# Performance work log

Hardware: AMD Instinct MI355X
Metric: run time of the kernel (lower is better)

Reference implementation:

```python
import jax, jax.numpy as jnp
import numpy as np

B, NV, NC, D, GD = 4, 2048, 8192, 64, 8


def setup_inputs() -> dict:
    key = jax.random.key(0)
    ks = jax.random.split(key, 16)
    f32 = jnp.float32
    rn = lambda k, s, fan: (jax.random.normal(k, s, dtype=f32) / np.float32(np.sqrt(fan)))
    raw = jax.random.randint(ks[0], (B, NC, NV), 0, 20)
    c_mat = jnp.where(raw == 0, -1.0, jnp.where(raw == 1, 1.0, 0.0)).astype(f32)
    v_mat = jnp.transpose(c_mat, (0, 2, 1))  # [B, NV, NC]
    variables = jax.random.normal(ks[1], (B, NV, D), dtype=f32)
    ground_vars = jax.random.normal(ks[2], (B, NV, GD), dtype=f32)
    # learned params
    c_block = rn(ks[3], (2, D, D), D)  # pos/neg literal projections (clause side)
    v_block = rn(ks[4], (2, D, D), D)  # pos/neg literal projections (variable side)
    vb = jax.random.normal(ks[5], (D,), dtype=f32)
    cb = jax.random.normal(ks[6], (D,), dtype=f32)
    Wg = rn(ks[7], (D, GD + D), GD + D)  # ground combiner Linear(concat) -> D
    bg = jnp.zeros((D,), f32)
    Wz = rn(ks[8], (D, D), D); Uz = rn(ks[9], (D, D), D); bz = jnp.zeros((D,), f32)
    Wr = rn(ks[10], (D, D), D); Ur = rn(ks[11], (D, D), D); br = jnp.zeros((D,), f32)
    Wh = rn(ks[12], (D, D), D); Uh = rn(ks[13], (D, D), D); bh = jnp.zeros((D,), f32)
    return dict(variables=variables, ground_vars=ground_vars, c_mat=c_mat, v_mat=v_mat,
                c_block=c_block, v_block=v_block, vb=vb, cb=cb, Wg=Wg, bg=bg,
                Wz=Wz, Uz=Uz, bz=bz, Wr=Wr, Ur=Ur, br=br, Wh=Wh, Uh=Uh, bh=bh)


def reference(variables, ground_vars, c_mat, v_mat, c_block, v_block, vb, cb,
              Wg, bg, Wz, Uz, bz, Wr, Ur, br, Wh, Uh, bh):
    b, nv, d = variables.shape
    v = variables.reshape(-1, d)  # [B*NV, D]
    # clause-side literal projections: bmm(c_block, v^T)^T == v @ c_block[i]^T
    pos_vars = (v @ c_block[0].T).reshape(b, nv, d)
    neg_vars = (v @ c_block[1].T).reshape(b, nv, d)
    pos_cmat = jnp.clip(c_mat, 0.0, 1.0)
    neg_cmat = -jnp.clip(c_mat, -1.0, 0.0)
    c = (jnp.einsum('bcv,bvd->bcd', pos_cmat, pos_vars)
         + jnp.einsum('bcv,bvd->bcd', neg_cmat, neg_vars))  # [B, NC, D]
    c = jax.nn.relu(c + cb)
    cv = c.reshape(-1, d)  # [B*NC, D]
    pos_cvars = (cv @ v_block[0].T).reshape(b, -1, d)
    neg_cvars = (cv @ v_block[1].T).reshape(b, -1, d)
    pos_vmat = jnp.clip(v_mat, 0.0, 1.0)
    neg_vmat = -jnp.clip(v_mat, -1.0, 0.0)
    nv_msg = (jnp.einsum('bvc,bcd->bvd', pos_vmat, pos_cvars)
              + jnp.einsum('bvc,bcd->bvd', neg_vmat, neg_cvars))  # [B, NV, D]
    v_emb = jax.nn.relu(nv_msg + vb).reshape(-1, d)
    # ground combiner: tanh(Linear(concat(ground, v_emb)))
    g = ground_vars.reshape(-1, ground_vars.shape[-1])
    av = jnp.tanh(jnp.concatenate([g, v_emb], axis=-1) @ Wg.T + bg)
    # GRU update against previous variable embeddings
    prev = v
    z = jax.nn.sigmoid(av @ Wz.T + prev @ Uz.T + bz)
    r = jax.nn.sigmoid(av @ Wr.T + prev @ Ur.T + br)
    h_tilda = jnp.tanh(av @ Wh.T + (r * prev) @ Uh.T + bh)
    h = (1.0 - z) * prev + z * h_tilda
    return h.reshape(b, nv * d, 1)
```

## Files before the change

### kernel.cpp

```cpp
#include <hip/hip_runtime.h>
#include <hip/hip_bf16.h>
#include <stdint.h>

#define NBATCH 4
#define NV 2048
#define NC 8192
#define DD 64

typedef __attribute__((ext_vector_type(8))) short s16x8;
typedef __attribute__((ext_vector_type(4))) float fx4;
typedef __attribute__((ext_vector_type(8))) unsigned short u16x8;
typedef __attribute__((ext_vector_type(4))) int i32x4;
typedef __attribute__((ext_vector_type(2))) unsigned int u32x2;

static __device__ __forceinline__ unsigned short bf16_rne(float x) {
    union { float f; unsigned int u; } v; v.f = x;
    unsigned int u = v.u;
    u += 0x7FFFu + ((u >> 16) & 1u);
    return (unsigned short)(u >> 16);
}
static __device__ __forceinline__ float bf16_f32(unsigned short h) {
    union { unsigned int u; float f; } v; v.u = ((unsigned int)h) << 16;
    return v.f;
}
static __device__ __forceinline__ void gload_lds16(const void* g, void* l) {
    __builtin_amdgcn_global_load_lds(
        (const __attribute__((address_space(1))) unsigned int*)g,
        (__attribute__((address_space(3))) unsigned int*)l, 16, 0, 0);
}

__global__ __launch_bounds__(256) void k_prep_pv(
    const float* __restrict__ vars, const float* __restrict__ cblk,
    char* __restrict__ qsh, char* __restrict__ qsl,
    char* __restrict__ qdh, char* __restrict__ qdl)
{
    __shared__ float sv[32][64];
    __shared__ float scb[2][64][65];
    int blk = blockIdx.x;
    int b = blk >> 6, ch = blk & 63;
    int t = threadIdx.x;
    const float* vsrc = vars + ((size_t)b * NV + (size_t)ch * 32) * DD;
    for (int i = t; i < 32 * 64; i += 256) sv[i >> 6][i & 63] = vsrc[i];
    for (int i = t; i < 2 * 64 * 64; i += 256) {
        int pn = i >> 12, dout = (i >> 6) & 63, k = i & 63;
        scb[pn][k][dout] = cblk[i];
    }
    __syncthreads();
    int ks = t >> 6, dout = t & 63;
    unsigned int wsh[2] = {0, 0}, wsl[2] = {0, 0}, wdh[2] = {0, 0}, wdl[2] = {0, 0};
    #pragma unroll
    for (int c8 = 0; c8 < 8; ++c8) {
        int vloc = ks * 8 + c8;
        float ap = 0.f, an = 0.f;
        for (int k = 0; k < 64; ++k) {
            float vv = sv[vloc][k];
            ap += vv * scb[0][k][dout];
            an += vv * scb[1][k][dout];
        }
        float s = (ap + an) * 0.5f, dv = (ap - an) * 0.5f;
        int qs_ = (int)rintf(s * 4096.f);
        int qd_ = (int)rintf(dv * 4096.f);
        qs_ = min(max(qs_, -32511), 32511);
        qd_ = min(max(qd_, -32511), 32511);
        int sh = (qs_ + 128) >> 8, sl = qs_ - (sh << 8);
        int dh = (qd_ + 128) >> 8, dl = qd_ - (dh << 8);
        int w = c8 >> 2, sft = (c8 & 3) * 8;
        wsh[w] |= (unsigned int)(sh & 0xFF) << sft;
        wsl[w] |= (unsigned int)(sl & 0xFF) << sft;
        wdh[w] |= (unsigned int)(dh & 0xFF) << sft;
        wdl[w] |= (unsigned int)(dl & 0xFF) << sft;
    }
    int kc = ch >> 1;
    int lg = ((ch & 1) << 1) | (ks >> 1);
    size_t off = (((size_t)(b * 32 + kc) * 64 + dout) * 4 + lg) * 16 + (ks & 1) * 8;
    *(u32x2*)(qsh + off) = (u32x2){wsh[0], wsh[1]};
    *(u32x2*)(qsl + off) = (u32x2){wsl[0], wsl[1]};
    *(u32x2*)(qdh + off) = (u32x2){wdh[0], wdh[1]};
    *(u32x2*)(qdl + off) = (u32x2){wdl[0], wdl[1]};
}

__global__ __launch_bounds__(256, 2) void k_phaseA(
    const float* __restrict__ cmat,
    const char* __restrict__ qsh, const char* __restrict__ qsl,
    const char* __restrict__ qdh, const char* __restrict__ qdl,
    float* __restrict__ cpart, unsigned short* __restrict__ comp)
{
    __shared__ char lds[2][16384];
    int blk = blockIdx.x;
    int combo = blk & 15;
    int rg = blk >> 4;
    int b = combo >> 2;
    int q = combo & 3;
    int t = threadIdx.x;
    int wv = t >> 6, l = t & 63, lr = l & 15, lg = l >> 4;
    int c0 = rg * 128 + wv * 32;
    const float* A0 = cmat + (size_t)b * NC * NV + (size_t)lr * NV + q * 512 + lg * 16;
    unsigned short* compb = comp + (size_t)b * 256 * NC;

    i32x4 ahi[2][4], alo[2][4];
    #pragma unroll
    for (int i = 0; i < 2; ++i)
        #pragma unroll
        for (int j = 0; j < 4; ++j) { ahi[i][j] = (i32x4){0,0,0,0}; alo[i][j] = (i32x4){0,0,0,0}; }

    {
        size_t gb = ((size_t)(b * 32 + q * 8)) * 4096 + (size_t)t * 16;
        char* lp = &lds[0][t * 16];
        gload_lds16(qsh + gb, lp);
        gload_lds16(qsl + gb, lp + 4096);
        gload_lds16(qdh + gb, lp + 8192);
        gload_lds16(qdl + gb, lp + 12288);
    }
    fx4 xc[2][4], xn[2][4];
    #pragma unroll
    for (int rt = 0; rt < 2; ++rt)
        #pragma unroll
        for (int j4 = 0; j4 < 4; ++j4)
            xc[rt][j4] = *(const fx4*)(A0 + (size_t)(c0 + rt * 16) * NV + j4 * 4);
    __syncthreads();

    int cur = 0;
    #pragma unroll 1
    for (int cc = 0; cc < 8; ++cc) {
        if (cc < 7) {
            size_t gb = ((size_t)(b * 32 + q * 8 + cc + 1)) * 4096 + (size_t)t * 16;
            char* lp = &lds[cur ^ 1][t * 16];
            gload_lds16(qsh + gb, lp);
            gload_lds16(qsl + gb, lp + 4096);
            gload_lds16(qdh + gb, lp + 8192);
            gload_lds16(qdl + gb, lp + 12288);
            #pragma unroll
            for (int rt = 0; rt < 2; ++rt)
                #pragma unroll
                for (int j4 = 0; j4 < 4; ++j4)
                    xn[rt][j4] = *(const fx4*)(A0 + (size_t)(c0 + rt * 16) * NV + (cc + 1) * 64 + j4 * 4);
        }
        i32x4 Asgn[2], Aabs[2];
        #pragma unroll
        for (int rt = 0; rt < 2; ++rt) {
            int tt[16];
            #pragma unroll
            for (int j = 0; j < 16; ++j) tt[j] = (int)xc[rt][j >> 2][j & 3];
            i32x4 sg;
            #pragma unroll
            for (int w = 0; w < 4; ++w)
                sg[w] = (unsigned int)(tt[4*w] & 0xFF) | ((unsigned int)(tt[4*w+1] & 0xFF) << 8)
                      | ((unsigned int)(tt[4*w+2] & 0xFF) << 16) | ((unsigned int)(tt[4*w+3] & 0xFF) << 24);
            Asgn[rt] = sg;
            i32x4 ab;
            #pragma unroll
            for (int w = 0; w < 4; ++w) ab[w] = sg[w] & 0x01010101;
            Aabs[rt] = ab;
            unsigned int b0 = 0, b1 = 0;
            #pragma unroll
            for (int j = 0; j < 8; ++j) b0 |= ((unsigned int)tt[j] & 3u) << (2 * j);
            #pragma unroll
            for (int j = 0; j < 8; ++j) b1 |= ((unsigned int)tt[8 + j] & 3u) << (2 * j);
            int v8 = q * 64 + cc * 8 + lg * 2;
            int crow = c0 + rt * 16 + lr;
            compb[(size_t)v8 * NC + crow] = (unsigned short)b0;
            compb[(size_t)(v8 + 1) * NC + crow] = (unsigned short)b1;
        }
        const char* bufp = lds[cur];
        #pragma unroll
        for (int n = 0; n < 4; ++n) {
            int boff = ((n * 16 + lr) * 4 + lg) * 16;
            i32x4 Bsh = *(const i32x4*)(bufp + boff);
            i32x4 Bsl = *(const i32x4*)(bufp + 4096 + boff);
            i32x4 Bdh = *(const i32x4*)(bufp + 8192 + boff);
            i32x4 Bdl = *(const i32x4*)(bufp + 12288 + boff);
            #pragma unroll
            for (int rt = 0; rt < 2; ++rt) {
                ahi[rt][n] = __builtin_amdgcn_mfma_i32_16x16x64_i8(Aabs[rt], Bsh, ahi[rt][n], 0, 0, 0);
                ahi[rt][n] = __builtin_amdgcn_mfma_i32_16x16x64_i8(Asgn[rt], Bdh, ahi[rt][n], 0, 0, 0);
                alo[rt][n] = __builtin_amdgcn_mfma_i32_16x16x64_i8(Aabs[rt], Bsl, alo[rt][n], 0, 0, 0);
                alo[rt][n] = __builtin_amdgcn_mfma_i32_16x16x64_i8(Asgn[rt], Bdl, alo[rt][n], 0, 0, 0);
            }
        }
        if (cc < 7) {
            #pragma unroll
            for (int rt = 0; rt < 2; ++rt)
                #pragma unroll
                for (int j4 = 0; j4 < 4; ++j4) xc[rt][j4] = xn[rt][j4];
        }
        __syncthreads();
        cur ^= 1;
    }
    float* dst = cpart + (((size_t)q * NBATCH + b) * NC + c0) * DD;
    #pragma unroll
    for (int rt = 0; rt < 2; ++rt)
        #pragma unroll
        for (int n = 0; n < 4; ++n)
            #pragma unroll
            for (int r = 0; r < 4; ++r) {
                float v = (float)(ahi[rt][n][r] * 256 + alo[rt][n][r]) * (1.0f / 4096.0f);
                dst[(size_t)(rt * 16 + lg * 4 + r) * DD + n * 16 + lr] = v;
            }
}

__global__ __launch_bounds__(256) void k_projC(
    const float* __restrict__ cpart, const float* __restrict__ cb,
    const float* __restrict__ vblk,
    unsigned short* __restrict__ csh, unsigned short* __restrict__ csl,
    unsigned short* __restrict__ cdh, unsigned short* __restrict__ cdl)
{
    __shared__ float src[32][64];
    __shared__ float svb[2][64][65];
    int blk = blockIdx.x;
    int b = blk >> 8, kc = blk & 255;
    int t = threadIdx.x;
    const size_t qs = (size_t)NBATCH * NC * DD;
    const float* cs = cpart + ((size_t)b * NC + (size_t)kc * 32) * DD;
    for (int i = t; i < 2048; i += 256) {
        int k = i & 63;
        float v = cb[k];
        #pragma unroll
        for (int p = 0; p < 4; ++p) v += cs[i + p * qs];
        src[i >> 6][k] = fmaxf(v, 0.f);
    }
    for (int i = t; i < 8192; i += 256) {
        int pn = i >> 12, dout = (i >> 6) & 63, k = i & 63;
        svb[pn][k][dout] = vblk[i];
    }
    __syncthreads();
    int ks = t >> 6, dout = t & 63;
    float ap[8] = {0.f, 0.f, 0.f, 0.f, 0.f, 0.f, 0.f, 0.f};
    float an[8] = {0.f, 0.f, 0.f, 0.f, 0.f, 0.f, 0.f, 0.f};
    for (int k = 0; k < 64; ++k) {
        float w0 = svb[0][k][dout], w1 = svb[1][k][dout];
        #pragma unroll
        for (int c8 = 0; c8 < 8; ++c8) {
            float rc = src[ks * 8 + c8][k];
            ap[c8] += rc * w0;
            an[c8] += rc * w1;
        }
    }
    u16x8 vsh, vsl, vdh, vdl;
    #pragma unroll
    for (int c8 = 0; c8 < 8; ++c8) {
        float s = (ap[c8] + an[c8]) * 0.5f, dv = (ap[c8] - an[c8]) * 0.5f;
        unsigned short h = bf16_rne(s);
        vsh[c8] = h; vsl[c8] = bf16_rne(s - bf16_f32(h));
        h = bf16_rne(dv);
        vdh[c8] = h; vdl[c8] = bf16_rne(dv - bf16_f32(h));
    }
    size_t obase = (size_t)b * NC * DD + (((size_t)kc * 4 + ks) * 64 + dout) * 8;
    *(u16x8*)(csh + obase) = vsh;
    *(u16x8*)(csl + obase) = vsl;
    *(u16x8*)(cdh + obase) = vdh;
    *(u16x8*)(cdl + obase) = vdl;
}

__global__ __launch_bounds__(256, 2) void k_phaseB(
    const unsigned short* __restrict__ comp,
    const unsigned short* __restrict__ csh, const unsigned short* __restrict__ csl,
    const unsigned short* __restrict__ cdh, const unsigned short* __restrict__ cdl,
    float* __restrict__ npart)
{
    __shared__ short lds[2][16384];
    int blk = blockIdx.x;
    int combo = blk & 63;
    int rg = blk >> 6;
    int b = combo >> 4;
    int q = combo & 15;
    int t = threadIdx.x;
    int wv = t >> 6, l = t & 63, lr = l & 15, lg = l >> 4;
    int v0 = rg * 256 + wv * 64;
    const unsigned short* compb = comp + (size_t)b * 256 * NC;
    const size_t cvb = (size_t)b * NC * DD;
    int sh_ = 2 * (lr & 7);
    const unsigned short* cp[4];
    #pragma unroll
    for (int rt = 0; rt < 4; ++rt)
        cp[rt] = compb + (size_t)((v0 + rt * 16 + lr) >> 3) * NC + q * 512 + lg * 8;

    fx4 acc[4][4];
    #pragma unroll
    for (int i = 0; i < 4; ++i)
        #pragma unroll
        for (int j = 0; j < 4; ++j) acc[i][j] = (fx4){0.f, 0.f, 0.f, 0.f};

    {
        size_t gb = cvb + (size_t)(q * 8) * 4096 + (size_t)t * 8;
        short* lp = &lds[0][t * 8];
        gload_lds16(csh + gb, lp);           gload_lds16(csh + gb + 2048, lp + 2048);
        gload_lds16(csl + gb, lp + 4096);    gload_lds16(csl + gb + 2048, lp + 6144);
        gload_lds16(cdh + gb, lp + 8192);    gload_lds16(cdh + gb + 2048, lp + 10240);
        gload_lds16(cdl + gb, lp + 12288);   gload_lds16(cdl + gb + 2048, lp + 14336);
    }
    u16x8 uc[4][2], un[4][2];
    #pragma unroll
    for (int rt = 0; rt < 4; ++rt) {
        uc[rt][0] = *(const u16x8*)(cp[rt]);
        uc[rt][1] = *(const u16x8*)(cp[rt] + 32);
    }
    __syncthreads();

    int cur = 0;
    #pragma unroll 1
    for (int cc = 0; cc < 8; ++cc) {
        if (cc < 7) {
            size_t gb = cvb + (size_t)(q * 8 + cc + 1) * 4096 + (size_t)t * 8;
            short* lp = &lds[cur ^ 1][t * 8];
            gload_lds16(csh + gb, lp);           gload_lds16(csh + gb + 2048, lp + 2048);
            gload_lds16(csl + gb, lp + 4096);    gload_lds16(csl + gb + 2048, lp + 6144);
            gload_lds16(cdh + gb, lp + 8192);    gload_lds16(cdh + gb + 2048, lp + 10240);
            gload_lds16(cdl + gb, lp + 12288);   gload_lds16(cdl + gb + 2048, lp + 14336);
            #pragma unroll
            for (int rt = 0; rt < 4; ++rt) {
                un[rt][0] = *(const u16x8*)(cp[rt] + (cc + 1) * 64);
                un[rt][1] = *(const u16x8*)(cp[rt] + (cc + 1) * 64 + 32);
            }
        }
        const short* bufp = &lds[cur][0];
        #pragma unroll
        for (int st = 0; st < 2; ++st) {
            s16x8 As[4], Aa[4];
            #pragma unroll
            for (int rt = 0; rt < 4; ++rt) {
                #pragma unroll
                for (int i = 0; i < 8; ++i) {
                    unsigned int tb = ((unsigned int)uc[rt][st][i] >> sh_) & 3u;
                    unsigned short m = (tb & 1u) ? (unsigned short)0x3F80 : (unsigned short)0;
                    As[rt][i] = (short)m;
                    Aa[rt][i] = (short)(m | ((tb & 2u) << 14));
                }
            }
            #pragma unroll
            for (int n = 0; n < 4; ++n) {
                int off = ((st * 4 + lg) * 64 + n * 16 + lr) * 8;
                s16x8 Bs0 = *(const s16x8*)(bufp + off);
                s16x8 Bs1 = *(const s16x8*)(bufp + 4096 + off);
                s16x8 Bd0 = *(const s16x8*)(bufp + 8192 + off);
                s16x8 Bd1 = *(const s16x8*)(bufp + 12288 + off);
                #pragma unroll
                for (int rt = 0; rt < 4; ++rt) {
                    acc[rt][n] = __builtin_amdgcn_mfma_f32_16x16x32_bf16(As[rt], Bs0, acc[rt][n], 0, 0, 0);
                    acc[rt][n] = __builtin_amdgcn_mfma_f32_16x16x32_bf16(As[rt], Bs1, acc[rt][n], 0, 0, 0);
                    acc[rt][n] = __builtin_amdgcn_mfma_f32_16x16x32_bf16(Aa[rt], Bd0, acc[rt][n], 0, 0, 0);
                    acc[rt][n] = __builtin_amdgcn_mfma_f32_16x16x32_bf16(Aa[rt], Bd1, acc[rt][n], 0, 0, 0);
                }
            }
        }
        if (cc < 7) {
            #pragma unroll
            for (int rt = 0; rt < 4; ++rt) { uc[rt][0] = un[rt][0]; uc[rt][1] = un[rt][1]; }
        }
        __syncthreads();
        cur ^= 1;
    }
    float* dst = npart + (((size_t)q * NBATCH + b) * NV + v0) * DD;
    #pragma unroll
    for (int rt = 0; rt < 4; ++rt)
        #pragma unroll
        for (int n = 0; n < 4; ++n)
            #pragma unroll
            for (int r = 0; r < 4; ++r)
                dst[(size_t)(rt * 16 + lg * 4 + r) * DD + n * 16 + lr] = acc[rt][n][r];
}

__global__ __launch_bounds__(512) void k_gru(
    const float* __restrict__ npart, const float* __restrict__ vars,
    const float* __restrict__ gv, const float* __restrict__ vb,
    const float* __restrict__ Wg, const float* __restrict__ bg,
    const float* __restrict__ Wz, const float* __restrict__ Uz, const float* __restrict__ bz,
    const float* __restrict__ Wr, const float* __restrict__ Ur, const float* __restrict__ brr,
    const float* __restrict__ Wh, const float* __restrict__ Uh, const float* __restrict__ bh,
    float* __restrict__ out)
{
    __shared__ float sWg[72][65];
    __shared__ float sWz[64][65], sUz[64][65];
    __shared__ float sWr[64][65], sUr[64][65];
    __shared__ float sWh[64][65], sUh[64][65];
    __shared__ float scat[8][72];
    __shared__ float sprev[8][64];
    __shared__ float sav[8][64];
    __shared__ float srp[8][64];
    int t = threadIdx.x;
    for (int i = t * 4; i < 4608; i += 2048) {
        fx4 g4 = *(const fx4*)(Wg + i);
        int dout = i / 72, j = i - dout * 72;
        #pragma unroll
        for (int jj = 0; jj < 4; ++jj) sWg[j + jj][dout] = g4[jj];
    }
    for (int i = t * 4; i < 4096; i += 2048) {
        int dout = i >> 6, k = i & 63;
        fx4 a;
        a = *(const fx4*)(Wz + i);
        #pragma unroll
        for (int jj = 0; jj < 4; ++jj) sWz[k + jj][dout] = a[jj];
        a = *(const fx4*)(Uz + i);
        #pragma unroll
        for (int jj = 0; jj < 4; ++jj) sUz[k + jj][dout] = a[jj];
        a = *(const fx4*)(Wr + i);
        #pragma unroll
        for (int jj = 0; jj < 4; ++jj) sWr[k + jj][dout] = a[jj];
        a = *(const fx4*)(Ur + i);
        #pragma unroll
        for (int jj = 0; jj < 4; ++jj) sUr[k + jj][dout] = a[jj];
        a = *(const fx4*)(Wh + i);
        #pragma unroll
        for (int jj = 0; jj < 4; ++jj) sWh[k + jj][dout] = a[jj];
        a = *(const fx4*)(Uh + i);
        #pragma unroll
        for (int jj = 0; jj < 4; ++jj) sUh[k + jj][dout] = a[jj];
    }
    int rr = t >> 6, dout = t & 63;
    const size_t qs = (size_t)NBATCH * NV * DD;
    #pragma unroll 1
    for (int it = 0; it < 4; ++it) {
        size_t row = (size_t)blockIdx.x * 32 + it * 8 + rr;
        float prev = vars[row * 64 + dout];
        float ve = vb[dout];
        #pragma unroll
        for (int s = 0; s < 16; ++s) ve += npart[(size_t)s * qs + row * 64 + dout];
        ve = fmaxf(ve, 0.f);
        scat[rr][8 + dout] = ve;
        if (dout < 8) scat[rr][dout] = gv[row * 8 + dout];
        sprev[rr][dout] = prev;
        __syncthreads();
        float a = bg[dout];
        for (int j = 0; j < 72; ++j) a += scat[rr][j] * sWg[j][dout];
        float av = 1.f - 2.f / (__expf(2.f * a) + 1.f);
        sav[rr][dout] = av;
        __syncthreads();
        float zi = bz[dout], ri = brr[dout], hwa = 0.f;
        for (int k = 0; k < 64; ++k) {
            float ak = sav[rr][k], pk = sprev[rr][k];
            zi += ak * sWz[k][dout] + pk * sUz[k][dout];
            ri += ak * sWr[k][dout] + pk * sUr[k][dout];
            hwa += ak * sWh[k][dout];
        }
        float z = 1.f / (1.f + __expf(-zi));
        float rgate = 1.f / (1.f + __expf(-ri));
        srp[rr][dout] = rgate * prev;
        __syncthreads();
        float hin = bh[dout] + hwa;
        for (int k = 0; k < 64; ++k) hin += srp[rr][k] * sUh[k][dout];
        float ht = 1.f - 2.f / (__expf(2.f * hin) + 1.f);
        out[row * 64 + dout] = (1.f - z) * prev + z * ht;
        __syncthreads();
    }
}

extern "C" void kernel_launch(void* const* d_in, const int* in_sizes, int n_in,
                              void* d_out, int out_size, void* d_ws, size_t ws_size,
                              hipStream_t stream) {
    (void)in_sizes; (void)n_in; (void)out_size; (void)ws_size;
    const float* vars = (const float*)d_in[0];
    const float* gv   = (const float*)d_in[1];
    const float* cmat = (const float*)d_in[2];
    const float* cblk = (const float*)d_in[4];
    const float* vblk = (const float*)d_in[5];
    const float* vb   = (const float*)d_in[6];
    const float* cb   = (const float*)d_in[7];
    const float* Wg   = (const float*)d_in[8];
    const float* bg   = (const float*)d_in[9];
    const float* Wz   = (const float*)d_in[10];
    const float* Uz   = (const float*)d_in[11];
    const float* bz   = (const float*)d_in[12];
    const float* Wr   = (const float*)d_in[13];
    const float* Ur   = (const float*)d_in[14];
    const float* br_  = (const float*)d_in[15];
    const float* Wh   = (const float*)d_in[16];
    const float* Uh   = (const float*)d_in[17];
    const float* bh   = (const float*)d_in[18];
    float* out = (float*)d_out;

    char* w = (char*)d_ws;
    const size_t MB = 1024 * 1024;
    char* qsh = w + 0 * MB;
    char* qsl = w + 1 * MB;
    char* qdh = w + 2 * MB;
    char* qdl = w + 3 * MB;
    unsigned short* csh = (unsigned short*)(w + 4 * MB);
    unsigned short* csl = (unsigned short*)(w + 8 * MB);
    unsigned short* cdh = (unsigned short*)(w + 12 * MB);
    unsigned short* cdl = (unsigned short*)(w + 16 * MB);
    float* cpart         = (float*)(w + 20 * MB);
    float* npart         = (float*)(w + 52 * MB);
    unsigned short* comp = (unsigned short*)(w + 84 * MB);

    k_prep_pv<<<256, 256, 0, stream>>>(vars, cblk, qsh, qsl, qdh, qdl);
    k_phaseA<<<1024, 256, 0, stream>>>(cmat, qsh, qsl, qdh, qdl, cpart, comp);
    k_projC<<<1024, 256, 0, stream>>>(cpart, cb, vblk, csh, csl, cdh, cdl);
    k_phaseB<<<512, 256, 0, stream>>>(comp, csh, csl, cdh, cdl, npart);
    k_gru<<<256, 512, 0, stream>>>(npart, vars, gv, vb, Wg, bg,
                                   Wz, Uz, bz, Wr, Ur, br_, Wh, Uh, bh, out);
}
```

Before: 166.4 us.

## Drop split-K in phase A and fuse bias+ReLU into its epilogue

Phase A now gives each block the full variable dimension (32 chunks) for one batch, with 8 waves of 16 rows each, instead of splitting K four ways. It writes the final clause activations with bias and ReLU applied. This removes the 4x partial-sum write and read-back and the reduction in k_projC. In exchange the grid shrinks from 1024 to 256 blocks with a longer serial loop, so there is less parallelism across the GPU and more B-tile reloads per block.

```diff
diff --git a/kernel.cpp b/kernel.cpp
--- a/kernel.cpp
+++ b/kernel.cpp
@@ -79,85 +79,74 @@
     *(u32x2*)(qdl + off) = (u32x2){wdl[0], wdl[1]};
 }
 
-__global__ __launch_bounds__(256, 2) void k_phaseA(
+__global__ __launch_bounds__(512, 4) void k_phaseA(
     const float* __restrict__ cmat,
     const char* __restrict__ qsh, const char* __restrict__ qsl,
     const char* __restrict__ qdh, const char* __restrict__ qdl,
-    float* __restrict__ cpart, unsigned short* __restrict__ comp)
+    const float* __restrict__ cb,
+    float* __restrict__ cfull, unsigned short* __restrict__ comp)
 {
     __shared__ char lds[2][16384];
     int blk = blockIdx.x;
-    int combo = blk & 15;
-    int rg = blk >> 4;
-    int b = combo >> 2;
-    int q = combo & 3;
+    int b = blk & 3;
+    int rg = blk >> 2;
     int t = threadIdx.x;
     int wv = t >> 6, l = t & 63, lr = l & 15, lg = l >> 4;
-    int c0 = rg * 128 + wv * 32;
-    const float* A0 = cmat + (size_t)b * NC * NV + (size_t)lr * NV + q * 512 + lg * 16;
+    int row0 = rg * 128 + wv * 16;
+    const float* A0 = cmat + (size_t)b * NC * NV + (size_t)(row0 + lr) * NV + lg * 16;
     unsigned short* compb = comp + (size_t)b * 256 * NC;
 
-    i32x4 ahi[2][4], alo[2][4];
-    #pragma unroll
-    for (int i = 0; i < 2; ++i)
-        #pragma unroll
-        for (int j = 0; j < 4; ++j) { ahi[i][j] = (i32x4){0,0,0,0}; alo[i][j] = (i32x4){0,0,0,0}; }
-
-    {
-        size_t gb = ((size_t)(b * 32 + q * 8)) * 4096 + (size_t)t * 16;
+    i32x4 ahi[4], alo[4];
+    #pragma unroll
+    for (int n = 0; n < 4; ++n) { ahi[n] = (i32x4){0,0,0,0}; alo[n] = (i32x4){0,0,0,0}; }
+
+    if (t < 256) {
+        size_t gb = ((size_t)(b * 32)) * 4096 + (size_t)t * 16;
         char* lp = &lds[0][t * 16];
         gload_lds16(qsh + gb, lp);
         gload_lds16(qsl + gb, lp + 4096);
         gload_lds16(qdh + gb, lp + 8192);
         gload_lds16(qdl + gb, lp + 12288);
     }
-    fx4 xc[2][4], xn[2][4];
-    #pragma unroll
-    for (int rt = 0; rt < 2; ++rt)
-        #pragma unroll
-        for (int j4 = 0; j4 < 4; ++j4)
-            xc[rt][j4] = *(const fx4*)(A0 + (size_t)(c0 + rt * 16) * NV + j4 * 4);
+    fx4 xc[4], xn[4];
+    #pragma unroll
+    for (int j4 = 0; j4 < 4; ++j4) xc[j4] = *(const fx4*)(A0 + j4 * 4);
     __syncthreads();
 
     int cur = 0;
     #pragma unroll 1
-    for (int cc = 0; cc < 8; ++cc) {
-        if (cc < 7) {
-            size_t gb = ((size_t)(b * 32 + q * 8 + cc + 1)) * 4096 + (size_t)t * 16;
-            char* lp = &lds[cur ^ 1][t * 16];
-            gload_lds16(qsh + gb, lp);
-            gload_lds16(qsl + gb, lp + 4096);
-            gload_lds16(qdh + gb, lp + 8192);
-            gload_lds16(qdl + gb, lp + 12288);
-            #pragma unroll
-            for (int rt = 0; rt < 2; ++rt)
-                #pragma unroll
-                for (int j4 = 0; j4 < 4; ++j4)
-                    xn[rt][j4] = *(const fx4*)(A0 + (size_t)(c0 + rt * 16) * NV + (cc + 1) * 64 + j4 * 4);
-        }
-        i32x4 Asgn[2], Aabs[2];
-        #pragma unroll
-        for (int rt = 0; rt < 2; ++rt) {
-            int tt[16];
-            #pragma unroll
-            for (int j = 0; j < 16; ++j) tt[j] = (int)xc[rt][j >> 2][j & 3];
-            i32x4 sg;
-            #pragma unroll
-            for (int w = 0; w < 4; ++w)
-                sg[w] = (unsigned int)(tt[4*w] & 0xFF) | ((unsigned int)(tt[4*w+1] & 0xFF) << 8)
-                      | ((unsigned int)(tt[4*w+2] & 0xFF) << 16) | ((unsigned int)(tt[4*w+3] & 0xFF) << 24);
-            Asgn[rt] = sg;
-            i32x4 ab;
-            #pragma unroll
-            for (int w = 0; w < 4; ++w) ab[w] = sg[w] & 0x01010101;
-            Aabs[rt] = ab;
+    for (int kc = 0; kc < 32; ++kc) {
+        if (kc < 31) {
+            if (t < 256) {
+                size_t gb = ((size_t)(b * 32 + kc + 1)) * 4096 + (size_t)t * 16;
+                char* lp = &lds[cur ^ 1][t * 16];
+                gload_lds16(qsh + gb, lp);
+                gload_lds16(qsl + gb, lp + 4096);
+                gload_lds16(qdh + gb, lp + 8192);
+                gload_lds16(qdl + gb, lp + 12288);
+            }
+            #pragma unroll
+            for (int j4 = 0; j4 < 4; ++j4)
+                xn[j4] = *(const fx4*)(A0 + (kc + 1) * 64 + j4 * 4);
+        }
+        int tt[16];
+        #pragma unroll
+        for (int j = 0; j < 16; ++j) tt[j] = (int)xc[j >> 2][j & 3];
+        i32x4 Asgn, Aabs;
+        #pragma unroll
+        for (int w = 0; w < 4; ++w)
+            Asgn[w] = (unsigned int)(tt[4*w] & 0xFF) | ((unsigned int)(tt[4*w+1] & 0xFF) << 8)
+                    | ((unsigned int)(tt[4*w+2] & 0xFF) << 16) | ((unsigned int)(tt[4*w+3] & 0xFF) << 24);
+        #pragma unroll
+        for (int w = 0; w < 4; ++w) Aabs[w] = Asgn[w] & 0x01010101;
+        {
             unsigned int b0 = 0, b1 = 0;
             #pragma unroll
             for (int j = 0; j < 8; ++j) b0 |= ((unsigned int)tt[j] & 3u) << (2 * j);
             #pragma unroll
             for (int j = 0; j < 8; ++j) b1 |= ((unsigned int)tt[8 + j] & 3u) << (2 * j);
-            int v8 = q * 64 + cc * 8 + lg * 2;
-            int crow = c0 + rt * 16 + lr;
+            int v8 = kc * 8 + lg * 2;
+            int crow = row0 + lr;
             compb[(size_t)v8 * NC + crow] = (unsigned short)b0;
             compb[(size_t)(v8 + 1) * NC + crow] = (unsigned short)b1;
         }
@@ -169,37 +158,33 @@
             i32x4 Bsl = *(const i32x4*)(bufp + 4096 + boff);
             i32x4 Bdh = *(const i32x4*)(bufp + 8192 + boff);
             i32x4 Bdl = *(const i32x4*)(bufp + 12288 + boff);
-            #pragma unroll
-            for (int rt = 0; rt < 2; ++rt) {
-                ahi[rt][n] = __builtin_amdgcn_mfma_i32_16x16x64_i8(Aabs[rt], Bsh, ahi[rt][n], 0, 0, 0);
-                ahi[rt][n] = __builtin_amdgcn_mfma_i32_16x16x64_i8(Asgn[rt], Bdh, ahi[rt][n], 0, 0, 0);
-                alo[rt][n] = __builtin_amdgcn_mfma_i32_16x16x64_i8(Aabs[rt], Bsl, alo[rt][n], 0, 0, 0);
-                alo[rt][n] = __builtin_amdgcn_mfma_i32_16x16x64_i8(Asgn[rt], Bdl, alo[rt][n], 0, 0, 0);
-            }
-        }
-        if (cc < 7) {
-            #pragma unroll
-            for (int rt = 0; rt < 2; ++rt)
-                #pragma unroll
-                for (int j4 = 0; j4 < 4; ++j4) xc[rt][j4] = xn[rt][j4];
+            ahi[n] = __builtin_amdgcn_mfma_i32_16x16x64_i8(Aabs, Bsh, ahi[n], 0, 0, 0);
+            ahi[n] = __builtin_amdgcn_mfma_i32_16x16x64_i8(Asgn, Bdh, ahi[n], 0, 0, 0);
+            alo[n] = __builtin_amdgcn_mfma_i32_16x16x64_i8(Aabs, Bsl, alo[n], 0, 0, 0);
+            alo[n] = __builtin_amdgcn_mfma_i32_16x16x64_i8(Asgn, Bdl, alo[n], 0, 0, 0);
+        }
+        if (kc < 31) {
+            #pragma unroll
+            for (int j4 = 0; j4 < 4; ++j4) xc[j4] = xn[j4];
         }
         __syncthreads();
         cur ^= 1;
     }
-    float* dst = cpart + (((size_t)q * NBATCH + b) * NC + c0) * DD;
-    #pragma unroll
-    for (int rt = 0; rt < 2; ++rt)
-        #pragma unroll
-        for (int n = 0; n < 4; ++n)
-            #pragma unroll
-            for (int r = 0; r < 4; ++r) {
-                float v = (float)(ahi[rt][n][r] * 256 + alo[rt][n][r]) * (1.0f / 4096.0f);
-                dst[(size_t)(rt * 16 + lg * 4 + r) * DD + n * 16 + lr] = v;
-            }
+    float* dst = cfull + ((size_t)b * NC + row0) * DD;
+    #pragma unroll
+    for (int n = 0; n < 4; ++n) {
+        int col = n * 16 + lr;
+        float cbv = cb[col];
+        #pragma unroll
+        for (int r = 0; r < 4; ++r) {
+            float v = (float)(ahi[n][r] * 256 + alo[n][r]) * (1.0f / 4096.0f) + cbv;
+            dst[(size_t)(lg * 4 + r) * DD + col] = fmaxf(v, 0.f);
+        }
+    }
 }
 
 __global__ __launch_bounds__(256) void k_projC(
-    const float* __restrict__ cpart, const float* __restrict__ cb,
+    const float* __restrict__ cfull,
     const float* __restrict__ vblk,
     unsigned short* __restrict__ csh, unsigned short* __restrict__ csl,
     unsigned short* __restrict__ cdh, unsigned short* __restrict__ cdl)
@@ -209,15 +194,8 @@
     int blk = blockIdx.x;
     int b = blk >> 8, kc = blk & 255;
     int t = threadIdx.x;
-    const size_t qs = (size_t)NBATCH * NC * DD;
-    const float* cs = cpart + ((size_t)b * NC + (size_t)kc * 32) * DD;
-    for (int i = t; i < 2048; i += 256) {
-        int k = i & 63;
-        float v = cb[k];
-        #pragma unroll
-        for (int p = 0; p < 4; ++p) v += cs[i + p * qs];
-        src[i >> 6][k] = fmaxf(v, 0.f);
-    }
+    const float* cs = cfull + ((size_t)b * NC + (size_t)kc * 32) * DD;
+    for (int i = t; i < 2048; i += 256) src[i >> 6][i & 63] = cs[i];
     for (int i = t; i < 8192; i += 256) {
         int pn = i >> 12, dout = (i >> 6) & 63, k = i & 63;
         svb[pn][k][dout] = vblk[i];
@@ -477,13 +455,13 @@
     unsigned short* csl = (unsigned short*)(w + 8 * MB);
     unsigned short* cdh = (unsigned short*)(w + 12 * MB);
     unsigned short* cdl = (unsigned short*)(w + 16 * MB);
-    float* cpart         = (float*)(w + 20 * MB);
-    float* npart         = (float*)(w + 52 * MB);
-    unsigned short* comp = (unsigned short*)(w + 84 * MB);
+    float* cfull         = (float*)(w + 20 * MB);
+    float* npart         = (float*)(w + 28 * MB);
+    unsigned short* comp = (unsigned short*)(w + 60 * MB);
 
     k_prep_pv<<<256, 256, 0, stream>>>(vars, cblk, qsh, qsl, qdh, qdl);
-    k_phaseA<<<1024, 256, 0, stream>>>(cmat, qsh, qsl, qdh, qdl, cpart, comp);
-    k_projC<<<1024, 256, 0, stream>>>(cpart, cb, vblk, csh, csl, cdh, cdl);
+    k_phaseA<<<256, 512, 0, stream>>>(cmat, qsh, qsl, qdh, qdl, cb, cfull, comp);
+    k_projC<<<1024, 256, 0, stream>>>(cfull, vblk, csh, csl, cdh, cdl);
     k_phaseB<<<512, 256, 0, stream>>>(comp, csh, csl, cdh, cdl, npart);
     k_gru<<<256, 512, 0, stream>>>(npart, vars, gv, vb, Wg, bg,
                                    Wz, Uz, bz, Wr, Ur, br_, Wh, Uh, bh, out);
```

New measurement: 175.5 us. 1.05x slower.

## Switch phase B from split-bf16 MFMA to split-int8 fixed-point MFMA

Applied to the files above, without the earlier changes.

The projected clause messages are quantized to 16-bit fixed point (scale 512) and split into high and low int8 bytes instead of hi/lo bf16 pairs. Phase B then uses i32 16x16x64 int8 MFMAs with signed/absolute adjacency bytes, halving the LDS/global bytes per step and doubling K per instruction. Each block now covers 128 variables instead of 256, with the grid doubled and occupancy raised to 4 blocks per SM. The fixed-point scale clamps and quantizes values, which risks accuracy loss if clause activations exceed the representable range or need finer resolution.

```diff
diff --git a/kernel.cpp b/kernel.cpp
--- a/kernel.cpp
+++ b/kernel.cpp
@@ -13,16 +13,6 @@
 typedef __attribute__((ext_vector_type(4))) int i32x4;
 typedef __attribute__((ext_vector_type(2))) unsigned int u32x2;
 
-static __device__ __forceinline__ unsigned short bf16_rne(float x) {
-    union { float f; unsigned int u; } v; v.f = x;
-    unsigned int u = v.u;
-    u += 0x7FFFu + ((u >> 16) & 1u);
-    return (unsigned short)(u >> 16);
-}
-static __device__ __forceinline__ float bf16_f32(unsigned short h) {
-    union { unsigned int u; float f; } v; v.u = ((unsigned int)h) << 16;
-    return v.f;
-}
 static __device__ __forceinline__ void gload_lds16(const void* g, void* l) {
     __builtin_amdgcn_global_load_lds(
         (const __attribute__((address_space(1))) unsigned int*)g,
@@ -201,16 +191,16 @@
 __global__ __launch_bounds__(256) void k_projC(
     const float* __restrict__ cpart, const float* __restrict__ cb,
     const float* __restrict__ vblk,
-    unsigned short* __restrict__ csh, unsigned short* __restrict__ csl,
-    unsigned short* __restrict__ cdh, unsigned short* __restrict__ cdl)
+    char* __restrict__ csh, char* __restrict__ csl,
+    char* __restrict__ cdh, char* __restrict__ cdl)
 {
     __shared__ float src[32][64];
     __shared__ float svb[2][64][65];
     int blk = blockIdx.x;
-    int b = blk >> 8, kc = blk & 255;
+    int b = blk >> 8, kc32 = blk & 255;
     int t = threadIdx.x;
     const size_t qs = (size_t)NBATCH * NC * DD;
-    const float* cs = cpart + ((size_t)b * NC + (size_t)kc * 32) * DD;
+    const float* cs = cpart + ((size_t)b * NC + (size_t)kc32 * 32) * DD;
     for (int i = t; i < 2048; i += 256) {
         int k = i & 63;
         float v = cb[k];
@@ -235,29 +225,38 @@
             an[c8] += rc * w1;
         }
     }
-    u16x8 vsh, vsl, vdh, vdl;
+    unsigned int wsh[2] = {0, 0}, wsl[2] = {0, 0}, wdh[2] = {0, 0}, wdl[2] = {0, 0};
     #pragma unroll
     for (int c8 = 0; c8 < 8; ++c8) {
         float s = (ap[c8] + an[c8]) * 0.5f, dv = (ap[c8] - an[c8]) * 0.5f;
-        unsigned short h = bf16_rne(s);
-        vsh[c8] = h; vsl[c8] = bf16_rne(s - bf16_f32(h));
-        h = bf16_rne(dv);
-        vdh[c8] = h; vdl[c8] = bf16_rne(dv - bf16_f32(h));
-    }
-    size_t obase = (size_t)b * NC * DD + (((size_t)kc * 4 + ks) * 64 + dout) * 8;
-    *(u16x8*)(csh + obase) = vsh;
-    *(u16x8*)(csl + obase) = vsl;
-    *(u16x8*)(cdh + obase) = vdh;
-    *(u16x8*)(cdl + obase) = vdl;
-}
-
-__global__ __launch_bounds__(256, 2) void k_phaseB(
+        int q_s = (int)rintf(s * 512.f);
+        int q_d = (int)rintf(dv * 512.f);
+        q_s = min(max(q_s, -32511), 32511);
+        q_d = min(max(q_d, -32511), 32511);
+        int sh = (q_s + 128) >> 8, sl = q_s - (sh << 8);
+        int dh = (q_d + 128) >> 8, dl = q_d - (dh << 8);
+        int w = c8 >> 2, sft = (c8 & 3) * 8;
+        wsh[w] |= (unsigned int)(sh & 0xFF) << sft;
+        wsl[w] |= (unsigned int)(sl & 0xFF) << sft;
+        wdh[w] |= (unsigned int)(dh & 0xFF) << sft;
+        wdl[w] |= (unsigned int)(dl & 0xFF) << sft;
+    }
+    int kc = kc32 >> 1;
+    int lgw = ((kc32 & 1) << 1) | (ks >> 1);
+    size_t off = (((size_t)(b * 128 + kc) * 64 + dout) * 4 + lgw) * 16 + (ks & 1) * 8;
+    *(u32x2*)(csh + off) = (u32x2){wsh[0], wsh[1]};
+    *(u32x2*)(csl + off) = (u32x2){wsl[0], wsl[1]};
+    *(u32x2*)(cdh + off) = (u32x2){wdh[0], wdh[1]};
+    *(u32x2*)(cdl + off) = (u32x2){wdl[0], wdl[1]};
+}
+
+__global__ __launch_bounds__(256, 4) void k_phaseB(
     const unsigned short* __restrict__ comp,
-    const unsigned short* __restrict__ csh, const unsigned short* __restrict__ csl,
-    const unsigned short* __restrict__ cdh, const unsigned short* __restrict__ cdl,
+    const char* __restrict__ csh, const char* __restrict__ csl,
+    const char* __restrict__ cdh, const char* __restrict__ cdl,
     float* __restrict__ npart)
 {
-    __shared__ short lds[2][16384];
+    __shared__ char lds[2][16384];
     int blk = blockIdx.x;
     int combo = blk & 63;
     int rg = blk >> 6;
@@ -265,98 +264,97 @@
     int q = combo & 15;
     int t = threadIdx.x;
     int wv = t >> 6, l = t & 63, lr = l & 15, lg = l >> 4;
-    int v0 = rg * 256 + wv * 64;
+    int v0 = rg * 128 + wv * 32;
     const unsigned short* compb = comp + (size_t)b * 256 * NC;
-    const size_t cvb = (size_t)b * NC * DD;
     int sh_ = 2 * (lr & 7);
-    const unsigned short* cp[4];
-    #pragma unroll
-    for (int rt = 0; rt < 4; ++rt)
-        cp[rt] = compb + (size_t)((v0 + rt * 16 + lr) >> 3) * NC + q * 512 + lg * 8;
-
-    fx4 acc[4][4];
-    #pragma unroll
-    for (int i = 0; i < 4; ++i)
-        #pragma unroll
-        for (int j = 0; j < 4; ++j) acc[i][j] = (fx4){0.f, 0.f, 0.f, 0.f};
+    const unsigned short* cp0 = compb + (size_t)((v0 + lr) >> 3) * NC + q * 512 + lg * 16;
+    const unsigned short* cp1 = compb + (size_t)((v0 + 16 + lr) >> 3) * NC + q * 512 + lg * 16;
+    const size_t cbase = ((size_t)(b * 128 + q * 8)) * 4096;
+
+    i32x4 ahi[2][4], alo[2][4];
+    #pragma unroll
+    for (int i = 0; i < 2; ++i)
+        #pragma unroll
+        for (int j = 0; j < 4; ++j) { ahi[i][j] = (i32x4){0,0,0,0}; alo[i][j] = (i32x4){0,0,0,0}; }
 
     {
-        size_t gb = cvb + (size_t)(q * 8) * 4096 + (size_t)t * 8;
-        short* lp = &lds[0][t * 8];
-        gload_lds16(csh + gb, lp);           gload_lds16(csh + gb + 2048, lp + 2048);
-        gload_lds16(csl + gb, lp + 4096);    gload_lds16(csl + gb + 2048, lp + 6144);
-        gload_lds16(cdh + gb, lp + 8192);    gload_lds16(cdh + gb + 2048, lp + 10240);
-        gload_lds16(cdl + gb, lp + 12288);   gload_lds16(cdl + gb + 2048, lp + 14336);
-    }
-    u16x8 uc[4][2], un[4][2];
-    #pragma unroll
-    for (int rt = 0; rt < 4; ++rt) {
-        uc[rt][0] = *(const u16x8*)(cp[rt]);
-        uc[rt][1] = *(const u16x8*)(cp[rt] + 32);
+        size_t gb = cbase + (size_t)t * 16;
+        char* lp = &lds[0][t * 16];
+        gload_lds16(csh + gb, lp);
+        gload_lds16(csl + gb, lp + 4096);
+        gload_lds16(cdh + gb, lp + 8192);
+        gload_lds16(cdl + gb, lp + 12288);
     }
     __syncthreads();
 
     int cur = 0;
     #pragma unroll 1
     for (int cc = 0; cc < 8; ++cc) {
+        u16x8 u00 = *(const u16x8*)(cp0 + cc * 64);
+        u16x8 u01 = *(const u16x8*)(cp0 + cc * 64 + 8);
+        u16x8 u10 = *(const u16x8*)(cp1 + cc * 64);
+        u16x8 u11 = *(const u16x8*)(cp1 + cc * 64 + 8);
         if (cc < 7) {
-            size_t gb = cvb + (size_t)(q * 8 + cc + 1) * 4096 + (size_t)t * 8;
-            short* lp = &lds[cur ^ 1][t * 8];
-            gload_lds16(csh + gb, lp);           gload_lds16(csh + gb + 2048, lp + 2048);
-            gload_lds16(csl + gb, lp + 4096);    gload_lds16(csl + gb + 2048, lp + 6144);
-            gload_lds16(cdh + gb, lp + 8192);    gload_lds16(cdh + gb + 2048, lp + 10240);
-            gload_lds16(cdl + gb, lp + 12288);   gload_lds16(cdl + gb + 2048, lp + 14336);
-            #pragma unroll
-            for (int rt = 0; rt < 4; ++rt) {
-                un[rt][0] = *(const u16x8*)(cp[rt] + (cc + 1) * 64);
-                un[rt][1] = *(const u16x8*)(cp[rt] + (cc + 1) * 64 + 32);
+            size_t gb = cbase + (size_t)(cc + 1) * 4096 + (size_t)t * 16;
+            char* lp = &lds[cur ^ 1][t * 16];
+            gload_lds16(csh + gb, lp);
+            gload_lds16(csl + gb, lp + 4096);
+            gload_lds16(cdh + gb, lp + 8192);
+            gload_lds16(cdl + gb, lp + 12288);
+        }
+        i32x4 Asgn[2], Aabs[2];
+        #pragma unroll
+        for (int rt = 0; rt < 2; ++rt) {
+            u16x8 ua = rt ? u10 : u00;
+            u16x8 ub = rt ? u11 : u01;
+            i32x4 sg;
+            #pragma unroll
+            for (int g = 0; g < 4; ++g) {
+                unsigned int wg = 0;
+                #pragma unroll
+                for (int jj = 0; jj < 4; ++jj) {
+                    int j = g * 4 + jj;
+                    unsigned int code = ((unsigned int)(j < 8 ? ua[j & 7] : ub[j & 7]) >> sh_) & 3u;
+                    unsigned int byt = (code == 3u) ? 0xFFu : code;
+                    wg |= byt << (jj * 8);
+                }
+                sg[g] = (int)wg;
             }
-        }
-        const short* bufp = &lds[cur][0];
-        #pragma unroll
-        for (int st = 0; st < 2; ++st) {
-            s16x8 As[4], Aa[4];
-            #pragma unroll
-            for (int rt = 0; rt < 4; ++rt) {
-                #pragma unroll
-                for (int i = 0; i < 8; ++i) {
-                    unsigned int tb = ((unsigned int)uc[rt][st][i] >> sh_) & 3u;
-                    unsigned short m = (tb & 1u) ? (unsigned short)0x3F80 : (unsigned short)0;
-                    As[rt][i] = (short)m;
-                    Aa[rt][i] = (short)(m | ((tb & 2u) << 14));
-                }
+            Asgn[rt] = sg;
+            i32x4 ab;
+            #pragma unroll
+            for (int g = 0; g < 4; ++g) ab[g] = sg[g] & 0x01010101;
+            Aabs[rt] = ab;
+        }
+        const char* bufp = lds[cur];
+        #pragma unroll
+        for (int n = 0; n < 4; ++n) {
+            int boff = ((n * 16 + lr) * 4 + lg) * 16;
+            i32x4 Bsh = *(const i32x4*)(bufp + boff);
+            i32x4 Bsl = *(const i32x4*)(bufp + 4096 + boff);
+            i32x4 Bdh = *(const i32x4*)(bufp + 8192 + boff);
+            i32x4 Bdl = *(const i32x4*)(bufp + 12288 + boff);
+            #pragma unroll
+            for (int rt = 0; rt < 2; ++rt) {
+                ahi[rt][n] = __builtin_amdgcn_mfma_i32_16x16x64_i8(Aabs[rt], Bsh, ahi[rt][n], 0, 0, 0);
+                ahi[rt][n] = __builtin_amdgcn_mfma_i32_16x16x64_i8(Asgn[rt], Bdh, ahi[rt][n], 0, 0, 0);
+                alo[rt][n] = __builtin_amdgcn_mfma_i32_16x16x64_i8(Aabs[rt], Bsl, alo[rt][n], 0, 0, 0);
+                alo[rt][n] = __builtin_amdgcn_mfma_i32_16x16x64_i8(Asgn[rt], Bdl, alo[rt][n], 0, 0, 0);
             }
-            #pragma unroll
-            for (int n = 0; n < 4; ++n) {
-                int off = ((st * 4 + lg) * 64 + n * 16 + lr) * 8;
-                s16x8 Bs0 = *(const s16x8*)(bufp + off);
-                s16x8 Bs1 = *(const s16x8*)(bufp + 4096 + off);
-                s16x8 Bd0 = *(const s16x8*)(bufp + 8192 + off);
-                s16x8 Bd1 = *(const s16x8*)(bufp + 12288 + off);
-                #pragma unroll
-                for (int rt = 0; rt < 4; ++rt) {
-                    acc[rt][n] = __builtin_amdgcn_mfma_f32_16x16x32_bf16(As[rt], Bs0, acc[rt][n], 0, 0, 0);
-                    acc[rt][n] = __builtin_amdgcn_mfma_f32_16x16x32_bf16(As[rt], Bs1, acc[rt][n], 0, 0, 0);
-                    acc[rt][n] = __builtin_amdgcn_mfma_f32_16x16x32_bf16(Aa[rt], Bd0, acc[rt][n], 0, 0, 0);
-                    acc[rt][n] = __builtin_amdgcn_mfma_f32_16x16x32_bf16(Aa[rt], Bd1, acc[rt][n], 0, 0, 0);
-                }
+        }
+        __syncthreads();
+        cur ^= 1;
+    }
+    float* dst = npart + (((size_t)q * NBATCH + b) * NV + v0) * DD;
+    #pragma unroll
+    for (int rt = 0; rt < 2; ++rt)
+        #pragma unroll
+        for (int n = 0; n < 4; ++n)
+            #pragma unroll
+            for (int r = 0; r < 4; ++r) {
+                float v = (float)(ahi[rt][n][r] * 256 + alo[rt][n][r]) * (1.0f / 512.0f);
+                dst[(size_t)(rt * 16 + lg * 4 + r) * DD + n * 16 + lr] = v;
             }
-        }
-        if (cc < 7) {
-            #pragma unroll
-            for (int rt = 0; rt < 4; ++rt) { uc[rt][0] = un[rt][0]; uc[rt][1] = un[rt][1]; }
-        }
-        __syncthreads();
-        cur ^= 1;
-    }
-    float* dst = npart + (((size_t)q * NBATCH + b) * NV + v0) * DD;
-    #pragma unroll
-    for (int rt = 0; rt < 4; ++rt)
-        #pragma unroll
-        for (int n = 0; n < 4; ++n)
-            #pragma unroll
-            for (int r = 0; r < 4; ++r)
-                dst[(size_t)(rt * 16 + lg * 4 + r) * DD + n * 16 + lr] = acc[rt][n][r];
 }
 
 __global__ __launch_bounds__(512) void k_gru(
@@ -473,18 +471,18 @@
     char* qsl = w + 1 * MB;
     char* qdh = w + 2 * MB;
     char* qdl = w + 3 * MB;
-    unsigned short* csh = (unsigned short*)(w + 4 * MB);
-    unsigned short* csl = (unsigned short*)(w + 8 * MB);
-    unsigned short* cdh = (unsigned short*)(w + 12 * MB);
-    unsigned short* cdl = (unsigned short*)(w + 16 * MB);
-    float* cpart         = (float*)(w + 20 * MB);
-    float* npart         = (float*)(w + 52 * MB);
-    unsigned short* comp = (unsigned short*)(w + 84 * MB);
+    char* csh = w + 4 * MB;
+    char* csl = w + 6 * MB;
+    char* cdh = w + 8 * MB;
+    char* cdl = w + 10 * MB;
+    float* cpart         = (float*)(w + 12 * MB);
+    float* npart         = (float*)(w + 44 * MB);
+    unsigned short* comp = (unsigned short*)(w + 76 * MB);
 
     k_prep_pv<<<256, 256, 0, stream>>>(vars, cblk, qsh, qsl, qdh, qdl);
     k_phaseA<<<1024, 256, 0, stream>>>(cmat, qsh, qsl, qdh, qdl, cpart, comp);
     k_projC<<<1024, 256, 0, stream>>>(cpart, cb, vblk, csh, csl, cdh, cdl);
-    k_phaseB<<<512, 256, 0, stream>>>(comp, csh, csl, cdh, cdl, npart);
+    k_phaseB<<<1024, 256, 0, stream>>>(comp, csh, csl, cdh, cdl, npart);
     k_gru<<<256, 512, 0, stream>>>(npart, vars, gv, vb, Wg, bg,
                                    Wz, Uz, bz, Wr, Ur, br_, Wh, Uh, bh, out);
 }
```

After: 165.4 us. Within noise of the previous version (-0.6%).
